# Kernel tuning notes

Hardware: AMD Instinct MI355X
Metric: run time of the kernel (lower is better)

Reference implementation:

```python
import jax
import jax.numpy as jnp
import numpy as np

IN_FEATS = 784
HIDDEN_DIM = 1024
BATCH = 1024


def setup_inputs() -> dict:
    key = jax.random.key(0)
    k_px, k_W, k_c, k_V, k_b = jax.random.split(key, 5)
    pixels = jax.random.uniform(k_px, (BATCH, IN_FEATS), dtype=jnp.float32)
    W = jax.random.normal(k_W, (HIDDEN_DIM, IN_FEATS), dtype=jnp.float32)
    c = jax.random.normal(k_c, (HIDDEN_DIM,), dtype=jnp.float32)
    V = jax.random.normal(k_V, (IN_FEATS, HIDDEN_DIM), dtype=jnp.float32)
    b = jax.random.normal(k_b, (IN_FEATS,), dtype=jnp.float32)
    return {"pixels": pixels, "W": W, "c": c, "V": V, "b": b}


def reference(pixels, W, c, V, b):
    # pixels: [B, D]; W: [H, D]; c: [H]; V: [D, H]; b: [D]
    B = pixels.shape[0]
    a0 = jnp.broadcast_to(c[None, :], (B, c.shape[0]))  # [B, H]

    def step(a, inp):
        w_col, v_row, b_i, x_i = inp  # [H], [H], [], [B]
        h = jax.nn.sigmoid(a)                     # [B, H]
        pred_i = b_i + h @ v_row                  # [B]
        a_next = a + w_col[None, :] * x_i[:, None]  # rank-1 accumulator update
        return a_next, pred_i

    xs = (W.T, V, b, pixels.T)  # each leading dim D (scan over visible units)
    _, preds = jax.lax.scan(step, a0, xs)  # preds: [D, B]
    return preds.T  # [B, D]
```

## Files before the change

### kernel.cpp

```cpp
#include <hip/hip_runtime.h>

#define B_ 1024
#define D_ 784
#define H_ 1024
#define BH_ (B_ * H_)
#define LOG2E 1.4426950408889634f


__global__ __launch_bounds__(256) void build_vw(const float* __restrict__ V,
                                                const float* __restrict__ W,
                                                float* __restrict__ VW) {
    __shared__ float t[32][33];
    int i0 = blockIdx.x * 32;
    int h0 = blockIdx.y * 32;
    int tx = threadIdx.x & 31, ty = threadIdx.x >> 5;
    int hb = h0 >> 8, hl = h0 & 255;
#pragma unroll
    for (int j = 0; j < 4; ++j) {
        int i = i0 + ty + j * 8;
        if (i < D_)
            VW[((size_t)i * 4 + hb) * 512 + hl + tx] = V[(size_t)i * H_ + h0 + tx];
    }
#pragma unroll
    for (int j = 0; j < 4; ++j) {
        int h = h0 + ty + j * 8;
        int i = i0 + tx;
        float v = 0.f;
        if (i < D_) v = W[(size_t)h * D_ + i] * LOG2E;
        t[ty + j * 8][tx] = v;
    }
    __syncthreads();
#pragma unroll
    for (int j = 0; j < 4; ++j) {
        int i = i0 + ty + j * 8;
        if (i < D_)
            VW[((size_t)i * 4 + hb) * 512 + 256 + hl + tx] = t[tx][ty + j * 8];
    }
}

__global__ __launch_bounds__(256) void prefix_gemm(const float* __restrict__ px,
                                                   const float* __restrict__ VW,
                                                   const float* __restrict__ c,
                                                   float* __restrict__ A0) {
    __shared__ float xs[8][64];
    __shared__ float ws[8][64];
    const int t = threadIdx.x;
    const int b0 = blockIdx.x * 64, h0 = blockIdx.y * 64;
    const int hbg = h0 >> 8, hlg = h0 & 255;
    const int tb = t >> 4, th = t & 15;

    float acc[4][4];
    float4 c4 = *(const float4*)(c + h0 + th * 4);
#pragma unroll
    for (int bi = 0; bi < 4; ++bi) {
        acc[bi][0] = c4.x * LOG2E; acc[bi][1] = c4.y * LOG2E;
        acc[bi][2] = c4.z * LOG2E; acc[bi][3] = c4.w * LOG2E;
    }
    const int xr = t >> 2, xc = (t & 3) * 2;

    for (int j0 = 0; j0 < 592; j0 += 8) {
        float2 xv = *(const float2*)(px + (size_t)(b0 + xr) * D_ + j0 + xc);
        float4 wv = make_float4(0, 0, 0, 0);
        if (t < 128)
            wv = *(const float4*)(VW + ((size_t)(j0 + (t >> 4)) * 4 + hbg) * 512 + 256 + hlg + (t & 15) * 4);
        __syncthreads();
        xs[xc][xr] = xv.x; xs[xc + 1][xr] = xv.y;
        if (t < 128) *(float4*)&ws[t >> 4][(t & 15) * 4] = wv;
        __syncthreads();
#pragma unroll
        for (int jj = 0; jj < 8; ++jj) {
            float4 xb = *(float4*)&xs[jj][tb * 4];
            float4 wb = *(float4*)&ws[jj][th * 4];
            float xa[4] = {xb.x, xb.y, xb.z, xb.w};
            float wa[4] = {wb.x, wb.y, wb.z, wb.w};
#pragma unroll
            for (int bi = 0; bi < 4; ++bi)
#pragma unroll
                for (int hi = 0; hi < 4; ++hi)
                    acc[bi][hi] = fmaf(xa[bi], wa[hi], acc[bi][hi]);
        }
        int jend = j0 + 8;
        if (jend == 200 || jend == 400 || jend == 592) {
            int sidx = (jend == 200) ? 0 : (jend == 400) ? 1 : 2;
            float* dst = A0 + (size_t)sidx * BH_;
#pragma unroll
            for (int bi = 0; bi < 4; ++bi) {
                float4 o = make_float4(acc[bi][0], acc[bi][1], acc[bi][2], acc[bi][3]);
                *(float4*)(dst + (size_t)(b0 + tb * 4 + bi) * H_ + h0 + th * 4) = o;
            }
        }
    }
}

template <int CTRL>
__device__ __forceinline__ float dpp_add(float p) {
    int s = __builtin_amdgcn_update_dpp(0, __float_as_int(p), CTRL, 0xf, 0xf, true);
    return p + __int_as_float(s);
}
__device__ __forceinline__ float reduce_halves(float p) {
    p = dpp_add<0x111>(p);
    p = dpp_add<0x112>(p);
    p = dpp_add<0x114>(p);
    p = dpp_add<0x118>(p);
    p = dpp_add<0x142>(p);
    return p;
}

__global__ __launch_bounds__(256, 8) void nade_main(
    const float* __restrict__ px,
    const float* __restrict__ c,
    const float* __restrict__ VW,
    const float* __restrict__ A0,
    float* __restrict__ part)
{
    const int lane = threadIdx.x & 63;
    const int wid  = threadIdx.x >> 6;
    const int gw   = blockIdx.x * 4 + wid;
    const int s    = gw & 3;
    const int hb   = (gw >> 2) & 3;
    const int rp   = gw >> 4;
    const int half = lane >> 5;
    const int row  = rp * 2 + half;
    const int hl   = lane & 31;
    const int h0   = hb * 256 + hl * 8;

    int i0s, i1s;
    if      (s == 0) { i0s = 0;   i1s = 200; }
    else if (s == 1) { i0s = 200; i1s = 400; }
    else if (s == 2) { i0s = 400; i1s = 592; }
    else             { i0s = 592; i1s = 784; }

    float A[8];
    if (s == 0) {
        float4 a0 = *(const float4*)(c + h0);
        float4 a1 = *(const float4*)(c + h0 + 4);
        A[0] = a0.x * LOG2E; A[1] = a0.y * LOG2E; A[2] = a0.z * LOG2E; A[3] = a0.w * LOG2E;
        A[4] = a1.x * LOG2E; A[5] = a1.y * LOG2E; A[6] = a1.z * LOG2E; A[7] = a1.w * LOG2E;
    } else {
        const float* ap = A0 + (size_t)(s - 1) * BH_ + (size_t)row * H_ + h0;
        float4 a0 = *(const float4*)(ap);
        float4 a1 = *(const float4*)(ap + 4);
        A[0] = a0.x; A[1] = a0.y; A[2] = a0.z; A[3] = a0.w;
        A[4] = a1.x; A[5] = a1.y; A[6] = a1.z; A[7] = a1.w;
    }

    const float* xp = px + (size_t)row * D_;
    float*       pp = part + ((size_t)hb * B_ + row) * D_;
    const float* vw = VW + ((size_t)i0s * 4 + hb) * 512 + hl * 8;

    auto grp4 = [&A](const float4& v4, const float4& w4, float xi, int k0) -> float {
        float e0 = __builtin_amdgcn_exp2f(fminf(30.f, -A[k0 + 0]));
        float e1 = __builtin_amdgcn_exp2f(fminf(30.f, -A[k0 + 1]));
        float e2 = __builtin_amdgcn_exp2f(fminf(30.f, -A[k0 + 2]));
        float e3 = __builtin_amdgcn_exp2f(fminf(30.f, -A[k0 + 3]));
        float q0 = 1.f + e0, q1 = 1.f + e1, q2 = 1.f + e2, q3 = 1.f + e3;
        float q01 = q0 * q1, q23 = q2 * q3;
        float r = __builtin_amdgcn_rcpf(q01 * q23);
        float t0 = v4.x * q1; t0 = fmaf(v4.y, q0, t0);
        float t1 = v4.z * q3; t1 = fmaf(v4.w, q2, t1);
        float n  = t0 * q23;  n  = fmaf(t1, q01, n);
        A[k0 + 0] = fmaf(w4.x, xi, A[k0 + 0]);
        A[k0 + 1] = fmaf(w4.y, xi, A[k0 + 1]);
        A[k0 + 2] = fmaf(w4.z, xi, A[k0 + 2]);
        A[k0 + 3] = fmaf(w4.w, xi, A[k0 + 3]);
        return n * r;
    };

    for (int ib = i0s; ib < i1s; ib += 4) {
        float4 xq = *(const float4*)(xp + ib);
        float xa[4] = {xq.x, xq.y, xq.z, xq.w};
        float pr[4];
#pragma unroll
        for (int j = 0; j < 4; ++j) {
            float4 v0 = *(const float4*)(vw + 0);
            float4 v1 = *(const float4*)(vw + 4);
            float4 w0 = *(const float4*)(vw + 256);
            float4 w1 = *(const float4*)(vw + 260);
            float p = grp4(v0, w0, xa[j], 0) + grp4(v1, w1, xa[j], 4);
            pr[j] = reduce_halves(p);
            vw += 2048;
        }
        if (hl == 31) {
            float4 o = make_float4(pr[0], pr[1], pr[2], pr[3]);
            *(float4*)(pp + ib) = o;
        }
    }
}

__global__ __launch_bounds__(256) void reduce_out(const float* __restrict__ part,
                                                  const float* __restrict__ bias,
                                                  float* __restrict__ out) {
    int t = blockIdx.x * 256 + threadIdx.x;
    if (t >= B_ * (D_ / 4)) return;
    int row = t / (D_ / 4);
    int ic  = (t - row * (D_ / 4)) * 4;
    float4 acc = *(const float4*)(bias + ic);
    const float* p = part + (size_t)row * D_ + ic;
#pragma unroll
    for (int hb = 0; hb < 4; ++hb) {
        float4 v = *(const float4*)(p + (size_t)hb * B_ * D_);
        acc.x += v.x; acc.y += v.y; acc.z += v.z; acc.w += v.w;
    }
    *(float4*)(out + (size_t)row * D_ + ic) = acc;
}

extern "C" void kernel_launch(void* const* d_in, const int* in_sizes, int n_in,
                              void* d_out, int out_size, void* d_ws, size_t ws_size,
                              hipStream_t stream) {
    const float* px   = (const float*)d_in[0];
    const float* W    = (const float*)d_in[1];
    const float* c    = (const float*)d_in[2];
    const float* V    = (const float*)d_in[3];
    const float* bias = (const float*)d_in[4];
    float* out = (float*)d_out;

    float* VW   = (float*)d_ws;
    float* A0   = VW + (size_t)D_ * 2048;
    float* part = A0 + (size_t)3 * BH_;

    build_vw<<<dim3((D_ + 31) / 32, H_ / 32), 256, 0, stream>>>(V, W, VW);
    prefix_gemm<<<dim3(B_ / 64, H_ / 64), 256, 0, stream>>>(px, VW, c, A0);

    nade_main<<<dim3(2048), 256, 0, stream>>>(px, c, VW, A0, part);

    reduce_out<<<dim3((B_ * (D_ / 4) + 255) / 256), 256, 0, stream>>>(part, bias, out);
}
```

Before: 348.0 us.

## Split scan into eight segments with per-segment GEMM partials fused into prep

The sequential scan over visible units is split into eight segments instead of four, doubling the number of waves in the main kernel and halving the serial chain length per wave. Segment starting accumulators are rebuilt in the main kernel by summing per-segment GEMM partials G, which are computed in parallel blocks fused into a single prep kernel alongside the VW layout build, removing one launch and the serial prefix GEMM. The VW layout is interleaved in pairs of rows and the sigmoid-weighted sum is fused over 8 hidden units with a single reciprocal. The exp clamp also drops from 30 to 15. The cost is more G traffic (7 slices written, up to 7 read per wave) and redundant prefix summing.

```diff
diff --git a/kernel.cpp b/kernel.cpp
--- a/kernel.cpp
+++ b/kernel.cpp
@@ -7,87 +7,103 @@
 #define LOG2E 1.4426950408889634f
 
 
-__global__ __launch_bounds__(256) void build_vw(const float* __restrict__ V,
-                                                const float* __restrict__ W,
-                                                float* __restrict__ VW) {
-    __shared__ float t[32][33];
-    int i0 = blockIdx.x * 32;
-    int h0 = blockIdx.y * 32;
-    int tx = threadIdx.x & 31, ty = threadIdx.x >> 5;
-    int hb = h0 >> 8, hl = h0 & 255;
-#pragma unroll
-    for (int j = 0; j < 4; ++j) {
-        int i = i0 + ty + j * 8;
-        if (i < D_)
-            VW[((size_t)i * 4 + hb) * 512 + hl + tx] = V[(size_t)i * H_ + h0 + tx];
-    }
-#pragma unroll
-    for (int j = 0; j < 4; ++j) {
-        int h = h0 + ty + j * 8;
-        int i = i0 + tx;
-        float v = 0.f;
-        if (i < D_) v = W[(size_t)h * D_ + i] * LOG2E;
-        t[ty + j * 8][tx] = v;
-    }
-    __syncthreads();
-#pragma unroll
-    for (int j = 0; j < 4; ++j) {
-        int i = i0 + ty + j * 8;
-        if (i < D_)
-            VW[((size_t)i * 4 + hb) * 512 + 256 + hl + tx] = t[tx][ty + j * 8];
-    }
-}
-
-__global__ __launch_bounds__(256) void prefix_gemm(const float* __restrict__ px,
-                                                   const float* __restrict__ VW,
-                                                   const float* __restrict__ c,
-                                                   float* __restrict__ A0) {
-    __shared__ float xs[8][64];
-    __shared__ float ws[8][64];
+__device__ __forceinline__ int seg_lo(int s) {
+    switch (s) {
+        case 0: return 0;   case 1: return 100; case 2: return 200; case 3: return 296;
+        case 4: return 396; case 5: return 492; case 6: return 592; default: return 688;
+    }
+}
+__device__ __forceinline__ int seg_hi(int s) {
+    switch (s) {
+        case 0: return 100; case 1: return 200; case 2: return 296; case 3: return 396;
+        case 4: return 492; case 5: return 592; case 6: return 688; default: return 784;
+    }
+}
+
+__global__ __launch_bounds__(256) void prep(const float* __restrict__ V,
+                                            const float* __restrict__ W,
+                                            const float* __restrict__ px,
+                                            float* __restrict__ VW,
+                                            float* __restrict__ G) {
+    __shared__ float smem[32 * 33];
     const int t = threadIdx.x;
-    const int b0 = blockIdx.x * 64, h0 = blockIdx.y * 64;
-    const int hbg = h0 >> 8, hlg = h0 & 255;
-    const int tb = t >> 4, th = t & 15;
-
-    float acc[4][4];
-    float4 c4 = *(const float4*)(c + h0 + th * 4);
-#pragma unroll
-    for (int bi = 0; bi < 4; ++bi) {
-        acc[bi][0] = c4.x * LOG2E; acc[bi][1] = c4.y * LOG2E;
-        acc[bi][2] = c4.z * LOG2E; acc[bi][3] = c4.w * LOG2E;
-    }
-    const int xr = t >> 2, xc = (t & 3) * 2;
-
-    for (int j0 = 0; j0 < 592; j0 += 8) {
-        float2 xv = *(const float2*)(px + (size_t)(b0 + xr) * D_ + j0 + xc);
-        float4 wv = make_float4(0, 0, 0, 0);
-        if (t < 128)
-            wv = *(const float4*)(VW + ((size_t)(j0 + (t >> 4)) * 4 + hbg) * 512 + 256 + hlg + (t & 15) * 4);
+
+    if (blockIdx.x < 800) {
+        int i0 = (blockIdx.x % 25) * 32;
+        int h0 = (blockIdx.x / 25) * 32;
+        int tx = t & 31, ty = t >> 5;
+#pragma unroll
+        for (int j = 0; j < 4; ++j) {
+            int i = i0 + ty + j * 8;
+            int h = h0 + tx;
+            if (i < D_)
+                VW[(size_t)(i >> 1) * 4096 + (h >> 8) * 1024 + (i & 1) * 512 + (h & 255)]
+                    = V[(size_t)i * H_ + h];
+        }
+#pragma unroll
+        for (int j = 0; j < 4; ++j) {
+            int h = h0 + ty + j * 8;
+            int i = i0 + tx;
+            float v = 0.f;
+            if (i < D_) v = W[(size_t)h * D_ + i] * LOG2E;
+            smem[(ty + j * 8) * 33 + tx] = v;
+        }
         __syncthreads();
-        xs[xc][xr] = xv.x; xs[xc + 1][xr] = xv.y;
-        if (t < 128) *(float4*)&ws[t >> 4][(t & 15) * 4] = wv;
-        __syncthreads();
-#pragma unroll
-        for (int jj = 0; jj < 8; ++jj) {
-            float4 xb = *(float4*)&xs[jj][tb * 4];
-            float4 wb = *(float4*)&ws[jj][th * 4];
-            float xa[4] = {xb.x, xb.y, xb.z, xb.w};
-            float wa[4] = {wb.x, wb.y, wb.z, wb.w};
-#pragma unroll
-            for (int bi = 0; bi < 4; ++bi)
-#pragma unroll
-                for (int hi = 0; hi < 4; ++hi)
-                    acc[bi][hi] = fmaf(xa[bi], wa[hi], acc[bi][hi]);
-        }
-        int jend = j0 + 8;
-        if (jend == 200 || jend == 400 || jend == 592) {
-            int sidx = (jend == 200) ? 0 : (jend == 400) ? 1 : 2;
-            float* dst = A0 + (size_t)sidx * BH_;
-#pragma unroll
-            for (int bi = 0; bi < 4; ++bi) {
-                float4 o = make_float4(acc[bi][0], acc[bi][1], acc[bi][2], acc[bi][3]);
-                *(float4*)(dst + (size_t)(b0 + tb * 4 + bi) * H_ + h0 + th * 4) = o;
+#pragma unroll
+        for (int j = 0; j < 4; ++j) {
+            int i = i0 + ty + j * 8;
+            int h = h0 + tx;
+            if (i < D_)
+                VW[(size_t)(i >> 1) * 4096 + (h >> 8) * 1024 + (i & 1) * 512 + 256 + (h & 255)]
+                    = smem[tx * 33 + ty + j * 8];
+        }
+    } else {
+        float* xs = smem;
+        float* ws = smem + 256;
+        int idx = blockIdx.x - 800;
+        int r   = idx >> 8;
+        int b0  = (idx & 15) * 64;
+        int h0  = ((idx >> 4) & 15) * 64;
+        int j0s = seg_lo(r), j1s = seg_hi(r);
+
+        const int tb = t >> 4, th = t & 15;
+        float acc[4][4];
+#pragma unroll
+        for (int bi = 0; bi < 4; ++bi)
+#pragma unroll
+            for (int hi = 0; hi < 4; ++hi) acc[bi][hi] = 0.f;
+
+        for (int j0 = j0s; j0 < j1s; j0 += 4) {
+            float xv = px[(size_t)(b0 + (t >> 2)) * D_ + j0 + (t & 3)];
+            float4 wv = make_float4(0, 0, 0, 0);
+            if (t < 64) wv = *(const float4*)(W + (size_t)(h0 + t) * D_ + j0);
+            __syncthreads();
+            xs[(t & 3) * 64 + (t >> 2)] = xv;
+            if (t < 64) {
+                ws[0 * 64 + t] = wv.x * LOG2E;
+                ws[1 * 64 + t] = wv.y * LOG2E;
+                ws[2 * 64 + t] = wv.z * LOG2E;
+                ws[3 * 64 + t] = wv.w * LOG2E;
             }
+            __syncthreads();
+#pragma unroll
+            for (int jj = 0; jj < 4; ++jj) {
+                float4 xb = *(float4*)&xs[jj * 64 + tb * 4];
+                float4 wb = *(float4*)&ws[jj * 64 + th * 4];
+                float xa[4] = {xb.x, xb.y, xb.z, xb.w};
+                float wa[4] = {wb.x, wb.y, wb.z, wb.w};
+#pragma unroll
+                for (int bi = 0; bi < 4; ++bi)
+#pragma unroll
+                    for (int hi = 0; hi < 4; ++hi)
+                        acc[bi][hi] = fmaf(xa[bi], wa[hi], acc[bi][hi]);
+            }
+        }
+        float* dst = G + (size_t)r * BH_;
+#pragma unroll
+        for (int bi = 0; bi < 4; ++bi) {
+            float4 o = make_float4(acc[bi][0], acc[bi][1], acc[bi][2], acc[bi][3]);
+            *(float4*)(dst + (size_t)(b0 + tb * 4 + bi) * H_ + h0 + th * 4) = o;
         }
     }
 }
@@ -110,59 +126,64 @@
     const float* __restrict__ px,
     const float* __restrict__ c,
     const float* __restrict__ VW,
-    const float* __restrict__ A0,
+    const float* __restrict__ G,
     float* __restrict__ part)
 {
     const int lane = threadIdx.x & 63;
     const int wid  = threadIdx.x >> 6;
     const int gw   = blockIdx.x * 4 + wid;
-    const int s    = gw & 3;
-    const int hb   = (gw >> 2) & 3;
-    const int rp   = gw >> 4;
+    const int s    = gw & 7;
+    const int hb   = (gw >> 3) & 3;
+    const int rp   = gw >> 5;
     const int half = lane >> 5;
     const int row  = rp * 2 + half;
     const int hl   = lane & 31;
     const int h0   = hb * 256 + hl * 8;
 
-    int i0s, i1s;
-    if      (s == 0) { i0s = 0;   i1s = 200; }
-    else if (s == 1) { i0s = 200; i1s = 400; }
-    else if (s == 2) { i0s = 400; i1s = 592; }
-    else             { i0s = 592; i1s = 784; }
+    const int i0s = seg_lo(s), i1s = seg_hi(s);
 
     float A[8];
-    if (s == 0) {
+    {
         float4 a0 = *(const float4*)(c + h0);
         float4 a1 = *(const float4*)(c + h0 + 4);
         A[0] = a0.x * LOG2E; A[1] = a0.y * LOG2E; A[2] = a0.z * LOG2E; A[3] = a0.w * LOG2E;
         A[4] = a1.x * LOG2E; A[5] = a1.y * LOG2E; A[6] = a1.z * LOG2E; A[7] = a1.w * LOG2E;
-    } else {
-        const float* ap = A0 + (size_t)(s - 1) * BH_ + (size_t)row * H_ + h0;
-        float4 a0 = *(const float4*)(ap);
-        float4 a1 = *(const float4*)(ap + 4);
-        A[0] = a0.x; A[1] = a0.y; A[2] = a0.z; A[3] = a0.w;
-        A[4] = a1.x; A[5] = a1.y; A[6] = a1.z; A[7] = a1.w;
+        for (int r = 0; r < s; ++r) {
+            const float* gp = G + (size_t)r * BH_ + (size_t)row * H_ + h0;
+            float4 g0 = *(const float4*)(gp);
+            float4 g1 = *(const float4*)(gp + 4);
+            A[0] += g0.x; A[1] += g0.y; A[2] += g0.z; A[3] += g0.w;
+            A[4] += g1.x; A[5] += g1.y; A[6] += g1.z; A[7] += g1.w;
+        }
     }
 
     const float* xp = px + (size_t)row * D_;
     float*       pp = part + ((size_t)hb * B_ + row) * D_;
-    const float* vw = VW + ((size_t)i0s * 4 + hb) * 512 + hl * 8;
-
-    auto grp4 = [&A](const float4& v4, const float4& w4, float xi, int k0) -> float {
-        float e0 = __builtin_amdgcn_exp2f(fminf(30.f, -A[k0 + 0]));
-        float e1 = __builtin_amdgcn_exp2f(fminf(30.f, -A[k0 + 1]));
-        float e2 = __builtin_amdgcn_exp2f(fminf(30.f, -A[k0 + 2]));
-        float e3 = __builtin_amdgcn_exp2f(fminf(30.f, -A[k0 + 3]));
-        float q0 = 1.f + e0, q1 = 1.f + e1, q2 = 1.f + e2, q3 = 1.f + e3;
-        float q01 = q0 * q1, q23 = q2 * q3;
-        float r = __builtin_amdgcn_rcpf(q01 * q23);
-        float t0 = v4.x * q1; t0 = fmaf(v4.y, q0, t0);
-        float t1 = v4.z * q3; t1 = fmaf(v4.w, q2, t1);
-        float n  = t0 * q23;  n  = fmaf(t1, q01, n);
-        A[k0 + 0] = fmaf(w4.x, xi, A[k0 + 0]);
-        A[k0 + 1] = fmaf(w4.y, xi, A[k0 + 1]);
-        A[k0 + 2] = fmaf(w4.z, xi, A[k0 + 2]);
-        A[k0 + 3] = fmaf(w4.w, xi, A[k0 + 3]);
+    const float* vwA = VW + (size_t)(i0s >> 1) * 4096 + hb * 1024 + hl * 8;
+    const float* vwB = vwA + 4096;
+
+    auto step8 = [&A](const float4& v0, const float4& v1,
+                      const float4& w0, const float4& w1, float xi) -> float {
+        float va[8] = {v0.x, v0.y, v0.z, v0.w, v1.x, v1.y, v1.z, v1.w};
+        float wa[8] = {w0.x, w0.y, w0.z, w0.w, w1.x, w1.y, w1.z, w1.w};
+        float q[8];
+#pragma unroll
+        for (int k = 0; k < 8; ++k) {
+            float e = __builtin_amdgcn_exp2f(fminf(15.f, -A[k]));
+            q[k] = 1.f + e;
+            A[k] = fmaf(wa[k], xi, A[k]);
+        }
+        float a01 = fmaf(va[0], q[1], va[1] * q[0]);
+        float a23 = fmaf(va[2], q[3], va[3] * q[2]);
+        float a45 = fmaf(va[4], q[5], va[5] * q[4]);
+        float a67 = fmaf(va[6], q[7], va[7] * q[6]);
+        float q01 = q[0] * q[1], q23 = q[2] * q[3];
+        float q45 = q[4] * q[5], q67 = q[6] * q[7];
+        float n0123 = fmaf(a01, q23, a23 * q01);
+        float n4567 = fmaf(a45, q67, a67 * q45);
+        float q0123 = q01 * q23, q4567 = q45 * q67;
+        float r = __builtin_amdgcn_rcpf(q0123 * q4567);
+        float n = fmaf(n0123, q4567, n4567 * q0123);
         return n * r;
     };
 
@@ -170,16 +191,27 @@
         float4 xq = *(const float4*)(xp + ib);
         float xa[4] = {xq.x, xq.y, xq.z, xq.w};
         float pr[4];
-#pragma unroll
-        for (int j = 0; j < 4; ++j) {
-            float4 v0 = *(const float4*)(vw + 0);
-            float4 v1 = *(const float4*)(vw + 4);
-            float4 w0 = *(const float4*)(vw + 256);
-            float4 w1 = *(const float4*)(vw + 260);
-            float p = grp4(v0, w0, xa[j], 0) + grp4(v1, w1, xa[j], 4);
-            pr[j] = reduce_halves(p);
-            vw += 2048;
-        }
+        {
+            float4 v0 = *(const float4*)(vwA + 0),   v1 = *(const float4*)(vwA + 4);
+            float4 w0 = *(const float4*)(vwA + 256), w1 = *(const float4*)(vwA + 260);
+            pr[0] = reduce_halves(step8(v0, v1, w0, w1, xa[0]));
+        }
+        {
+            float4 v0 = *(const float4*)(vwA + 512), v1 = *(const float4*)(vwA + 516);
+            float4 w0 = *(const float4*)(vwA + 768), w1 = *(const float4*)(vwA + 772);
+            pr[1] = reduce_halves(step8(v0, v1, w0, w1, xa[1]));
+        }
+        {
+            float4 v0 = *(const float4*)(vwB + 0),   v1 = *(const float4*)(vwB + 4);
+            float4 w0 = *(const float4*)(vwB + 256), w1 = *(const float4*)(vwB + 260);
+            pr[2] = reduce_halves(step8(v0, v1, w0, w1, xa[2]));
+        }
+        {
+            float4 v0 = *(const float4*)(vwB + 512), v1 = *(const float4*)(vwB + 516);
+            float4 w0 = *(const float4*)(vwB + 768), w1 = *(const float4*)(vwB + 772);
+            pr[3] = reduce_halves(step8(v0, v1, w0, w1, xa[3]));
+        }
+        vwA += 8192; vwB += 8192;
         if (hl == 31) {
             float4 o = make_float4(pr[0], pr[1], pr[2], pr[3]);
             *(float4*)(pp + ib) = o;
@@ -215,13 +247,12 @@
     float* out = (float*)d_out;
 
     float* VW   = (float*)d_ws;
-    float* A0   = VW + (size_t)D_ * 2048;
-    float* part = A0 + (size_t)3 * BH_;
-
-    build_vw<<<dim3((D_ + 31) / 32, H_ / 32), 256, 0, stream>>>(V, W, VW);
-    prefix_gemm<<<dim3(B_ / 64, H_ / 64), 256, 0, stream>>>(px, VW, c, A0);
-
-    nade_main<<<dim3(2048), 256, 0, stream>>>(px, c, VW, A0, part);
+    float* G    = VW + (size_t)392 * 4096;
+    float* part = G + (size_t)7 * BH_;
+
+    prep<<<dim3(2592), 256, 0, stream>>>(V, W, px, VW, G);
+
+    nade_main<<<dim3(4096), 256, 0, stream>>>(px, c, VW, G, part);
 
     reduce_out<<<dim3((B_ * (D_ / 4) + 255) / 256), 256, 0, stream>>>(part, bias, out);
 }
```

New measurement: 375.2 us. 7.8% more time.
